# Performance work log

Measured on AMD Instinct MI355X. Metric: run time of the kernel, lower is better.

## Reference

```python
import jax, jax.numpy as jnp
import numpy as np

# Fixed architecture constants (match init_kwargs)
D_MODEL = 256
NHEAD = 8
BASE_WINDOW = 4
DFF = 1024
B = 1
S = 4096


def _win_idx(grid, w):
    """Token indices of overlapping w x w windows over a grid x grid image,
    stride w//2 (same windows as F.unfold(kernel=w, stride=w//2)). -> (L, w*w) int32."""
    s = w // 2
    starts = np.arange(0, grid - w + 1, s)
    rows = starts[:, None] + np.arange(w)[None, :]              # (n, w)
    idx = rows[:, None, :, None] * grid + rows[None, :, None, :]  # (n, n, w, w)
    return jnp.asarray(idx.reshape(-1, w * w), dtype=jnp.int32)


def _ln(x, g, b, eps=1e-5):
    m = jnp.mean(x, axis=-1, keepdims=True)
    v = jnp.var(x, axis=-1, keepdims=True)
    return (x - m) * jax.lax.rsqrt(v + eps) * g + b


def _local_attn(x, scale, fw, fb, fg, fbb):
    """Multi-scale windowed SDPA: gather windows, attend, mean-pool per window,
    scatter pooled features back to token positions (overlap-averaged), fuse."""
    Bq, Sq, Dm = x.shape
    grid = int(np.sqrt(Sq))
    inv_scale = 1.0 / float(np.sqrt(Dm))  # SDPA uses full D as head dim
    outs = []
    for i in range(3):
        w = BASE_WINDOW * (2 ** i) * scale
        idx = _win_idx(grid, w)                      # (L, w2)
        win = x[:, idx, :]                           # (B, L, w2, D) gather
        p = jax.nn.softmax(jnp.einsum('blqd,blkd->blqk', win, win) * inv_scale, axis=-1)
        pooled = jnp.einsum('blqk,blkd->blqd', p, win).mean(axis=2)  # (B, L, D)
        flat = idx.reshape(-1)
        contrib = jnp.broadcast_to(pooled[:, :, None, :], win.shape).reshape(Bq, -1, Dm)
        acc = jnp.zeros_like(x).at[:, flat, :].add(contrib)
        cnt = jnp.zeros((Sq,), x.dtype).at[flat].add(1.0)
        outs.append(acc / cnt[None, :, None])        # (B, S, D) per scale
    cat = jnp.concatenate(outs, axis=-1)             # (B, S, 3D)
    return _ln(cat @ fw + fb, fg, fbb)


def _mha(x, wq, wk, wv, bq, bk, bv, wo, bo):
    Bq, Sq, Dm = x.shape
    dh = Dm // NHEAD
    def split(t):
        return t.reshape(Bq, Sq, NHEAD, dh)
    q, k, v = split(x @ wq + bq), split(x @ wk + bk), split(x @ wv + bv)
    p = jax.nn.softmax(jnp.einsum('bqhd,bkhd->bhqk', q, k) * (1.0 / float(np.sqrt(dh))), axis=-1)
    o = jnp.einsum('bhqk,bkhd->bqhd', p, v).reshape(Bq, Sq, Dm)
    return o @ wo + bo


def _forward(x, pos, fw, fb, fg, fbb, wq, wk, wv, bq, bk, bv, wo, bo, gw, gb, w1, b1, w2, b2, n1g, n1b, n2g, n2b, n3g, n3b, local_scale):
    # pos is accepted but unused in the original math (device check only)
    xl = _local_attn(x, local_scale, fw, fb, fg, fbb)
    xl = _ln(x + xl, n1g, n1b)                 # norm1 residual (dropout is identity in eval)
    xg = _mha(xl, wq, wk, wv, bq, bk, bv, wo, bo)
    xg = _ln(xl + xg, n2g, n2b)                # norm2 residual
    gate = jax.nn.softmax(((xl + xg) * 0.5).mean(axis=1, keepdims=True) @ gw + gb, axis=-1)  # (B,1,2)
    alpha, beta = gate[..., 0:1], gate[..., 1:2]
    xf = alpha * xg + beta * xl
    ff = jax.nn.gelu(xf @ w1 + b1, approximate=False) @ w2 + b2
    return _ln(xf + ff, n3g, n3b)


def setup_inputs() -> dict:
    key = jax.random.key(0)
    ks = jax.random.split(key, 12)
    def rn(k, shape, s=0.02):
        return jax.random.normal(k, shape, jnp.float32) * s
    D = D_MODEL
    return {
        'x': jax.random.normal(ks[0], (B, S, D), jnp.float32),
        'pos': jax.random.normal(ks[1], (B, S, 2), jnp.float32),
        'fw': rn(ks[2], (3 * D, D)), 'fb': jnp.zeros((D,), jnp.float32),
        'fg': jnp.ones((D,), jnp.float32), 'fbb': jnp.zeros((D,), jnp.float32),
        'wq': rn(ks[3], (D, D)), 'wk': rn(ks[4], (D, D)), 'wv': rn(ks[5], (D, D)),
        'bq': jnp.zeros((D,), jnp.float32), 'bk': jnp.zeros((D,), jnp.float32), 'bv': jnp.zeros((D,), jnp.float32),
        'wo': rn(ks[6], (D, D)), 'bo': jnp.zeros((D,), jnp.float32),
        'gw': rn(ks[7], (D, 2)), 'gb': jnp.zeros((2,), jnp.float32),
        'w1': rn(ks[8], (D, DFF)), 'b1': jnp.zeros((DFF,), jnp.float32),
        'w2': rn(ks[9], (DFF, D)), 'b2': jnp.zeros((D,), jnp.float32),
        'n1g': jnp.ones((D,), jnp.float32), 'n1b': jnp.zeros((D,), jnp.float32),
        'n2g': jnp.ones((D,), jnp.float32), 'n2b': jnp.zeros((D,), jnp.float32),
        'n3g': jnp.ones((D,), jnp.float32), 'n3b': jnp.zeros((D,), jnp.float32),
        'local_scale': 1,
    }


def reference(x, pos, fw, fb, fg, fbb, wq, wk, wv, bq, bk, bv, wo, bo, gw, gb, w1, b1, w2, b2, n1g, n1b, n2g, n2b, n3g, n3b, local_scale):
    return _forward(x, pos, fw, fb, fg, fbb, wq, wk, wv, bq, bk, bv, wo, bo, gw, gb, w1, b1, w2, b2, n1g, n1b, n2g, n2b, n3g, n3b, local_scale)
```

## Files before the change

### kernel.cpp

```cpp
#include <hip/hip_runtime.h>
#include <hip/hip_bf16.h>
#include <cstdint>
#include <cstddef>


#define DEVFN __device__ __forceinline__

constexpr int S    = 4096;
constexpr int D    = 256;
constexpr int GRID = 64;
constexpr int NH   = 8;
constexpr int DH   = 32;

typedef __attribute__((ext_vector_type(8))) short bf16x8;
typedef __attribute__((ext_vector_type(4))) float f32x4;
typedef __attribute__((ext_vector_type(16))) float f32x16;
typedef __attribute__((ext_vector_type(2))) unsigned int u32x2;

DEVFN float asf(unsigned u) { return __uint_as_float(u); }

DEVFN unsigned short f2bf(float f) {
  unsigned u = __float_as_uint(f);
  u += 0x7fffu + ((u >> 16) & 1u);
  return (unsigned short)(u >> 16);
}
DEVFN float bf2f(unsigned short s) { return __uint_as_float(((unsigned)s) << 16); }

DEVFN unsigned pk2(float a, float b) {
  __hip_bfloat162 h = __float22bfloat162_rn(make_float2(a, b));
  return *(unsigned*)&h;
}

DEVFN bf16x8 pack8(float4 a, float4 b) {
  union { unsigned w[4]; bf16x8 v; } u;
  u.w[0] = pk2(a.x, a.y); u.w[1] = pk2(a.z, a.w);
  u.w[2] = pk2(b.x, b.y); u.w[3] = pk2(b.z, b.w);
  return u.v;
}

DEVFN float ex2(float x) {
#if __has_builtin(__builtin_amdgcn_exp2f)
  return __builtin_amdgcn_exp2f(x);
#else
  return __expf(x * 0.6931471805599453f);
#endif
}

DEVFN float gelu_t(float u) {
  const float y = 0.7978845608028654f * (u + 0.044715f * u * u * u);
  const float e = __expf(2.f * y);
  return 0.5f * u * (2.f - 2.f / (e + 1.f));
}

__global__ __launch_bounds__(256) void k_wt(
    const float* fw, const float* wq, const float* wk, const float* wv,
    const float* wo, const float* w1, const float* w2,
    unsigned short* fwT, unsigned short* wqT, unsigned short* wkT,
    unsigned short* wvT, unsigned short* woT, unsigned short* w1T,
    unsigned short* w2T) {
  __shared__ unsigned short tile[32][36];
  const int bid = blockIdx.x;
  const float* src; unsigned short* dst; int K, N, t;
  if (bid < 192)      { src = fw; dst = fwT; K = 768;  N = 256;  t = bid; }
  else if (bid < 256) { src = wq; dst = wqT; K = 256;  N = 256;  t = bid - 192; }
  else if (bid < 320) { src = wk; dst = wkT; K = 256;  N = 256;  t = bid - 256; }
  else if (bid < 384) { src = wv; dst = wvT; K = 256;  N = 256;  t = bid - 320; }
  else if (bid < 448) { src = wo; dst = woT; K = 256;  N = 256;  t = bid - 384; }
  else if (bid < 704) { src = w1; dst = w1T; K = 256;  N = 1024; t = bid - 448; }
  else                { src = w2; dst = w2T; K = 1024; N = 256;  t = bid - 704; }
  const int nkt = K >> 5;
  const int k0 = (t % nkt) * 32, n0 = (t / nkt) * 32;
  const int i = threadIdx.x >> 3, j4 = threadIdx.x & 7;
  const float4 v = *(const float4*)(src + (size_t)(k0 + i) * N + n0 + j4 * 4);
  *(uint2*)&tile[i][j4 * 4] = make_uint2(pk2(v.x, v.y), pk2(v.z, v.w));
  __syncthreads();
  unsigned o0 = tile[j4 * 4 + 0][i], o1 = tile[j4 * 4 + 1][i];
  unsigned o2 = tile[j4 * 4 + 2][i], o3 = tile[j4 * 4 + 3][i];
  *(uint2*)(dst + (size_t)(n0 + i) * K + k0 + j4 * 4) =
      make_uint2(o0 | (o1 << 16), o2 | (o3 << 16));
}

template <int K, int OUTBF, int ACT>
__global__ __launch_bounds__(64) void k_gemm_m(const unsigned short* __restrict__ Ab,
                                               const unsigned short* __restrict__ WT,
                                               const float* __restrict__ bias,
                                               void* __restrict__ Cout, int N) {
  const int lane = threadIdx.x;
  const int lc = lane & 31, hi = lane >> 5;
  const int m0 = blockIdx.x * 32, n0 = blockIdx.y * 32;
  const unsigned short* ap = Ab + (size_t)(m0 + lc) * K + hi * 8;
  const unsigned short* bp = WT + (size_t)(n0 + lc) * K + hi * 8;
  f32x16 acc0 = {0.f,0.f,0.f,0.f,0.f,0.f,0.f,0.f,0.f,0.f,0.f,0.f,0.f,0.f,0.f,0.f};
  f32x16 acc1 = acc0;
#pragma unroll 4
  for (int k0 = 0; k0 < K; k0 += 32) {
    bf16x8 a0 = *(const bf16x8*)(ap + k0);
    bf16x8 b0 = *(const bf16x8*)(bp + k0);
    bf16x8 a1 = *(const bf16x8*)(ap + k0 + 16);
    bf16x8 b1 = *(const bf16x8*)(bp + k0 + 16);
    acc0 = __builtin_amdgcn_mfma_f32_32x32x16_bf16(a0, b0, acc0, 0, 0, 0);
    acc1 = __builtin_amdgcn_mfma_f32_32x32x16_bf16(a1, b1, acc1, 0, 0, 0);
  }
  const float bv = bias[n0 + lc];
#pragma unroll
  for (int r = 0; r < 16; ++r) {
    const int row = (r & 3) + 8 * (r >> 2) + 4 * hi;
    float v = acc0[r] + acc1[r] + bv;
    if (ACT == 1) v = gelu_t(v);
    if (OUTBF) ((unsigned short*)Cout)[(size_t)(m0 + row) * N + n0 + lc] = f2bf(v);
    else       ((float*)Cout)[(size_t)(m0 + row) * N + n0 + lc] = v;
  }
}

__global__ __launch_bounds__(64) void k_gemm_qkv(const unsigned short* __restrict__ Ab,
                                                 const unsigned short* __restrict__ wqkvT,
                                                 const float* __restrict__ bq,
                                                 const float* __restrict__ bk,
                                                 const float* __restrict__ bv,
                                                 unsigned short* __restrict__ qb,
                                                 unsigned short* __restrict__ kb,
                                                 unsigned short* __restrict__ vb) {
  const int lane = threadIdx.x;
  const int lc = lane & 31, hi = lane >> 5;
  const int m0 = blockIdx.x * 32;
  const int sel = blockIdx.y >> 3, n0 = (blockIdx.y & 7) * 32;
  const unsigned short* WT = wqkvT + (size_t)sel * 256 * 256;
  const float* bias = sel == 0 ? bq : sel == 1 ? bk : bv;
  unsigned short* out = sel == 0 ? qb : sel == 1 ? kb : vb;
  const float oscale = sel == 0 ? 0.25505889254f : 1.f;
  const unsigned short* ap = Ab + (size_t)(m0 + lc) * 256 + hi * 8;
  const unsigned short* bp = WT + (size_t)(n0 + lc) * 256 + hi * 8;
  f32x16 acc0 = {0.f,0.f,0.f,0.f,0.f,0.f,0.f,0.f,0.f,0.f,0.f,0.f,0.f,0.f,0.f,0.f};
  f32x16 acc1 = acc0;
#pragma unroll 4
  for (int k0 = 0; k0 < 256; k0 += 32) {
    bf16x8 a0 = *(const bf16x8*)(ap + k0);
    bf16x8 b0 = *(const bf16x8*)(bp + k0);
    bf16x8 a1 = *(const bf16x8*)(ap + k0 + 16);
    bf16x8 b1 = *(const bf16x8*)(bp + k0 + 16);
    acc0 = __builtin_amdgcn_mfma_f32_32x32x16_bf16(a0, b0, acc0, 0, 0, 0);
    acc1 = __builtin_amdgcn_mfma_f32_32x32x16_bf16(a1, b1, acc1, 0, 0, 0);
  }
  const float bvv = bias[n0 + lc];
#pragma unroll
  for (int r = 0; r < 16; ++r) {
    const int row = (r & 3) + 8 * (r >> 2) + 4 * hi;
    out[(size_t)(m0 + row) * 256 + n0 + lc] = f2bf((acc0[r] + acc1[r] + bvv) * oscale);
  }
}

template <int W, int THREADS>
__global__ __launch_bounds__(THREADS) void k_local_s(const float* __restrict__ x,
                                                     float* __restrict__ pooled, int nS) {
  constexpr int NT  = W * W;
  constexpr int NCT = NT / 16;
  constexpr int LDE = 264;
  __shared__ unsigned short win[NT][LDE];
  __shared__ float a[NT];
  const int tid = threadIdx.x;
  const int wave = tid >> 6, lane = tid & 63;
  const int lr = lane & 15, lg = lane >> 4;
  const int l = blockIdx.x;
  const int row0 = (l / nS) * (W / 2), col0 = (l % nS) * (W / 2);

  for (int e8 = tid; e8 < NT * 32; e8 += THREADS) {
    const int t = e8 >> 5, c8 = (e8 & 31) * 8;
    const float* src = x + ((size_t)((row0 + t / W) * GRID + col0 + (t % W))) * D + c8;
    *(bf16x8*)&win[t][c8] = pack8(*(const float4*)src, *(const float4*)(src + 4));
  }
  if (tid < NT) a[tid] = 0.f;
  __syncthreads();

  bf16x8 af[8];
#pragma unroll
  for (int k2 = 0; k2 < 8; ++k2)
    af[k2] = *(const bf16x8*)&win[wave * 16 + lr][k2 * 32 + lg * 8];

  float m[4], Z[4], Zi[4];
#pragma unroll
  for (int r = 0; r < 4; ++r) { m[r] = -INFINITY; Z[r] = 0.f; }

  for (int ct = 0; ct < NCT; ++ct) {
    f32x4 Ca = {0.f, 0.f, 0.f, 0.f}, Cb = {0.f, 0.f, 0.f, 0.f};
#pragma unroll
    for (int k2 = 0; k2 < 8; k2 += 2) {
      bf16x8 b0 = *(const bf16x8*)&win[ct * 16 + lr][k2 * 32 + lg * 8];
      bf16x8 b1 = *(const bf16x8*)&win[ct * 16 + lr][(k2 + 1) * 32 + lg * 8];
      Ca = __builtin_amdgcn_mfma_f32_16x16x32_bf16(af[k2], b0, Ca, 0, 0, 0);
      Cb = __builtin_amdgcn_mfma_f32_16x16x32_bf16(af[k2 + 1], b1, Cb, 0, 0, 0);
    }
#pragma unroll
    for (int r = 0; r < 4; ++r) {
      const float sv = (Ca[r] + Cb[r]) * 0.0625f;
      const float nm = fmaxf(m[r], sv);
      Z[r] = Z[r] * __expf(m[r] - nm) + __expf(sv - nm);
      m[r] = nm;
    }
  }
#pragma unroll
  for (int r = 0; r < 4; ++r) {
#pragma unroll
    for (int msk = 1; msk <= 8; msk <<= 1) {
      const float om = __shfl_xor(m[r], msk), oz = __shfl_xor(Z[r], msk);
      const float nm = fmaxf(m[r], om);
      Z[r] = Z[r] * __expf(m[r] - nm) + oz * __expf(om - nm);
      m[r] = nm;
    }
    Zi[r] = 1.f / Z[r];
  }

  for (int ct = 0; ct < NCT; ++ct) {
    f32x4 Ca = {0.f, 0.f, 0.f, 0.f}, Cb = {0.f, 0.f, 0.f, 0.f};
#pragma unroll
    for (int k2 = 0; k2 < 8; k2 += 2) {
      bf16x8 b0 = *(const bf16x8*)&win[ct * 16 + lr][k2 * 32 + lg * 8];
      bf16x8 b1 = *(const bf16x8*)&win[ct * 16 + lr][(k2 + 1) * 32 + lg * 8];
      Ca = __builtin_amdgcn_mfma_f32_16x16x32_bf16(af[k2], b0, Ca, 0, 0, 0);
      Cb = __builtin_amdgcn_mfma_f32_16x16x32_bf16(af[k2 + 1], b1, Cb, 0, 0, 0);
    }
    float cs = 0.f;
#pragma unroll
    for (int r = 0; r < 4; ++r)
      cs += __expf((Ca[r] + Cb[r]) * 0.0625f - m[r]) * Zi[r];
    cs += __shfl_xor(cs, 16);
    cs += __shfl_xor(cs, 32);
    if (lg == 0) atomicAdd(&a[ct * 16 + lr], cs);
  }
  __syncthreads();

  for (int d = tid; d < D; d += THREADS) {
    float acc = 0.f;
#pragma unroll 8
    for (int k = 0; k < NT; ++k) acc += a[k] * bf2f(win[k][d]);
    pooled[(size_t)l * D + d] = acc * (1.f / NT);
  }
}

__global__ __launch_bounds__(256, 1) void k_local16(const float* __restrict__ x,
                                                    float* __restrict__ pooled, int nS) {
  constexpr int LDE = 264;
  __shared__ unsigned short win[256][LDE];
  __shared__ float a[256];
  const int tid = threadIdx.x;
  const int wave = tid >> 6, lane = tid & 63;
  const int lc = lane & 31, hi = lane >> 5;
  const int l = blockIdx.x;
  const int row0 = (l / nS) * 8, col0 = (l % nS) * 8;

  for (int e8 = tid; e8 < 256 * 32; e8 += 256) {
    const int t = e8 >> 5, c8 = (e8 & 31) * 8;
    const float* src = x + ((size_t)((row0 + (t >> 4)) * GRID + col0 + (t & 15))) * D + c8;
    *(bf16x8*)&win[t][c8] = pack8(*(const float4*)src, *(const float4*)(src + 4));
  }
  a[tid] = 0.f;
  __syncthreads();

  float m[2][16], Z[2][16], Zi[2][16];
#pragma unroll
  for (int s = 0; s < 2; ++s)
#pragma unroll
    for (int r = 0; r < 16; ++r) { m[s][r] = -INFINITY; Z[s][r] = 0.f; }

#pragma unroll
  for (int s = 0; s < 2; ++s) {
    const int R0 = (wave * 2 + s) * 32;
    bf16x8 af[16];
#pragma unroll
    for (int k2 = 0; k2 < 16; ++k2)
      af[k2] = *(const bf16x8*)&win[R0 + lc][k2 * 16 + hi * 8];
    for (int ct = 0; ct < 8; ++ct) {
      f32x16 Ca = {0.f,0.f,0.f,0.f,0.f,0.f,0.f,0.f,0.f,0.f,0.f,0.f,0.f,0.f,0.f,0.f};
      f32x16 Cb = Ca;
#pragma unroll
      for (int k2 = 0; k2 < 16; k2 += 2) {
        bf16x8 b0 = *(const bf16x8*)&win[ct * 32 + lc][k2 * 16 + hi * 8];
        bf16x8 b1 = *(const bf16x8*)&win[ct * 32 + lc][(k2 + 1) * 16 + hi * 8];
        Ca = __builtin_amdgcn_mfma_f32_32x32x16_bf16(af[k2], b0, Ca, 0, 0, 0);
        Cb = __builtin_amdgcn_mfma_f32_32x32x16_bf16(af[k2 + 1], b1, Cb, 0, 0, 0);
      }
#pragma unroll
      for (int r = 0; r < 16; ++r) {
        const float sv = (Ca[r] + Cb[r]) * 0.0625f;
        const float nm = fmaxf(m[s][r], sv);
        Z[s][r] = Z[s][r] * __expf(m[s][r] - nm) + __expf(sv - nm);
        m[s][r] = nm;
      }
    }
#pragma unroll
    for (int r = 0; r < 16; ++r) {
#pragma unroll
      for (int msk = 1; msk <= 16; msk <<= 1) {
        const float om = __shfl_xor(m[s][r], msk), oz = __shfl_xor(Z[s][r], msk);
        const float nm = fmaxf(m[s][r], om);
        Z[s][r] = Z[s][r] * __expf(m[s][r] - nm) + oz * __expf(om - nm);
        m[s][r] = nm;
      }
      Zi[s][r] = 1.f / Z[s][r];
    }
  }

#pragma unroll
  for (int s = 0; s < 2; ++s) {
    const int R0 = (wave * 2 + s) * 32;
    bf16x8 af[16];
#pragma unroll
    for (int k2 = 0; k2 < 16; ++k2)
      af[k2] = *(const bf16x8*)&win[R0 + lc][k2 * 16 + hi * 8];
    for (int ct = 0; ct < 8; ++ct) {
      f32x16 Ca = {0.f,0.f,0.f,0.f,0.f,0.f,0.f,0.f,0.f,0.f,0.f,0.f,0.f,0.f,0.f,0.f};
      f32x16 Cb = Ca;
#pragma unroll
      for (int k2 = 0; k2 < 16; k2 += 2) {
        bf16x8 b0 = *(const bf16x8*)&win[ct * 32 + lc][k2 * 16 + hi * 8];
        bf16x8 b1 = *(const bf16x8*)&win[ct * 32 + lc][(k2 + 1) * 16 + hi * 8];
        Ca = __builtin_amdgcn_mfma_f32_32x32x16_bf16(af[k2], b0, Ca, 0, 0, 0);
        Cb = __builtin_amdgcn_mfma_f32_32x32x16_bf16(af[k2 + 1], b1, Cb, 0, 0, 0);
      }
      float cs = 0.f;
#pragma unroll
      for (int r = 0; r < 16; ++r)
        cs += __expf((Ca[r] + Cb[r]) * 0.0625f - m[s][r]) * Zi[s][r];
      cs += __shfl_xor(cs, 32);
      if (hi == 0) atomicAdd(&a[ct * 32 + lc], cs);
    }
  }
  __syncthreads();

  {
    const int d = tid;
    float acc = 0.f;
#pragma unroll 8
    for (int k = 0; k < 256; ++k) acc += a[k] * bf2f(win[k][d]);
    pooled[(size_t)l * D + d] = acc * (1.f / 256.f);
  }
}

DEVFN float gatherp(const float* __restrict__ pooled, int r, int c, int W, int s, int nS, int d) {
  int amin = max(0, (r - W + s) / s), amax = min(nS - 1, r / s);
  int bmin = max(0, (c - W + s) / s), bmax = min(nS - 1, c / s);
  float acc = 0.f;
  int cnt = 0;
  for (int a = amin; a <= amax; ++a)
    for (int b = bmin; b <= bmax; ++b) { acc += pooled[(size_t)(a * nS + b) * D + d]; ++cnt; }
  return acc / (float)cnt;
}

__global__ void k_combine(const float* __restrict__ p0, const float* __restrict__ p1,
                          const float* __restrict__ p2, unsigned short* __restrict__ catb) {
  const int t = blockIdx.x, d = threadIdx.x;
  const int r = t >> 6, c = t & 63;
  unsigned short* o = catb + (size_t)t * 768;
  o[d]       = f2bf(gatherp(p0, r, c, 4, 2, 31, d));
  o[256 + d] = f2bf(gatherp(p1, r, c, 8, 4, 15, d));
  o[512 + d] = f2bf(gatherp(p2, r, c, 16, 8, 7, d));
}

DEVFN float2 block_sum2(float a, float b) {
  __shared__ float sb[8];
#pragma unroll
  for (int m = 32; m; m >>= 1) { a += __shfl_xor(a, m); b += __shfl_xor(b, m); }
  const int w = threadIdx.x >> 6;
  __syncthreads();
  if ((threadIdx.x & 63) == 0) { sb[w] = a; sb[4 + w] = b; }
  __syncthreads();
  return make_float2(sb[0] + sb[1] + sb[2] + sb[3], sb[4] + sb[5] + sb[6] + sb[7]);
}

__global__ __launch_bounds__(256) void k_ln(float* __restrict__ out, unsigned short* __restrict__ outb,
                                            const float* __restrict__ a, const float* __restrict__ b,
                                            const float* __restrict__ g, const float* __restrict__ be) {
  const size_t i = (size_t)blockIdx.x * D + threadIdx.x;
  float v = a[i] + (b ? b[i] : 0.f);
  float2 s = block_sum2(v, v * v);
  float mean = s.x * (1.f / D);
  float var = s.y * (1.f / D) - mean * mean;
  const float r = (v - mean) * rsqrtf(var + 1e-5f) * g[threadIdx.x] + be[threadIdx.x];
  out[i] = r;
  if (outb) outb[i] = f2bf(r);
}

__global__ __launch_bounds__(256) void k_ln_fuse(const float* __restrict__ t1,
                                                 const float* __restrict__ x,
                                                 float* __restrict__ xl,
                                                 unsigned short* __restrict__ xlb,
                                                 const float* __restrict__ fg,
                                                 const float* __restrict__ fbb,
                                                 const float* __restrict__ n1g,
                                                 const float* __restrict__ n1b) {
  const size_t i = (size_t)blockIdx.x * D + threadIdx.x;
  const float v1 = t1[i];
  float2 s1 = block_sum2(v1, v1 * v1);
  const float mean1 = s1.x * (1.f / D);
  const float var1 = s1.y * (1.f / D) - mean1 * mean1;
  const float r1 = (v1 - mean1) * rsqrtf(var1 + 1e-5f) * fg[threadIdx.x] + fbb[threadIdx.x];
  const float v2 = x[i] + r1;
  float2 s2 = block_sum2(v2, v2 * v2);
  const float mean2 = s2.x * (1.f / D);
  const float var2 = s2.y * (1.f / D) - mean2 * mean2;
  const float r2 = (v2 - mean2) * rsqrtf(var2 + 1e-5f) * n1g[threadIdx.x] + n1b[threadIdx.x];
  xl[i] = r2;
  xlb[i] = f2bf(r2);
}

__global__ __launch_bounds__(256) void k_flash_mfma(const unsigned short* __restrict__ Qg,
                                                    const unsigned short* __restrict__ Kg,
                                                    const unsigned short* __restrict__ Vg,
                                                    unsigned short* __restrict__ po,
                                                    float* __restrict__ pml) {
  const int h = blockIdx.y, z = blockIdx.z;
  const int tid = threadIdx.x;
  const int wave = tid >> 6, lane = tid & 63;
  const int lr = lane & 15, lg = lane >> 4;
  constexpr int NT2 = 16;

  __shared__ unsigned short Kf[2][64][40];
  __shared__ unsigned short VS[2][2048];

  const int q0 = blockIdx.x * 64 + wave * 16;
  const int kbase = z * 1024;

  const bf16x8 qfrag = *(const bf16x8*)(Qg + (size_t)(q0 + lr) * D + h * DH + lg * 8);

  f32x4 o0 = {0.f, 0.f, 0.f, 0.f}, o1 = {0.f, 0.f, 0.f, 0.f};
  float mrow = -INFINITY, lrow = 0.f;

  const unsigned vsbase0 =
      (unsigned)(unsigned long long)(const void*)&VS[0][0] + (unsigned)(lg * 128 + lr * 2);

  const int key = tid >> 2, c8 = (tid & 3) * 8;
  const int vidx = (c8 >> 4) * 1024 + (key >> 2) * 64 + (key & 3) * 16 + (c8 & 15);
  const unsigned short* kp = Kg + (size_t)(kbase + key) * D + h * DH + c8;
  const unsigned short* vp = Vg + (size_t)(kbase + key) * D + h * DH + c8;
  constexpr int KSTEP = 64 * D;

  {
    bf16x8 k0r = *(const bf16x8*)kp;
    bf16x8 v0r = *(const bf16x8*)vp;
    *(bf16x8*)&Kf[0][key][c8] = k0r;
    *(bf16x8*)&VS[0][vidx] = v0r;
  }
  __syncthreads();

  for (int kt = 0; kt < NT2; ++kt) {
    const int cur = kt & 1;
    const int ktn = (kt + 1 < NT2) ? kt + 1 : kt;
    bf16x8 kreg = *(const bf16x8*)(kp + (size_t)ktn * KSTEP);
    bf16x8 vreg = *(const bf16x8*)(vp + (size_t)ktn * KSTEP);

    f32x4 s[4];
    __builtin_amdgcn_s_setprio(1);
#pragma unroll
    for (int k16 = 0; k16 < 4; ++k16) {
      bf16x8 ka = *(const bf16x8*)&Kf[cur][k16 * 16 + lr][lg * 8];
      f32x4 zc = {0.f, 0.f, 0.f, 0.f};
      s[k16] = __builtin_amdgcn_mfma_f32_16x16x32_bf16(ka, qfrag, zc, 0, 0, 0);
    }
    __builtin_amdgcn_s_setprio(0);

    const unsigned vb = vsbase0 + (unsigned)(cur << 12);
    u32x2 tv000, tv001, tv010, tv011, tv100, tv101, tv110, tv111;
    asm volatile("ds_read_b64_tr_b16 %0, %1 offset:0"    : "=v"(tv000) : "v"(vb));
    asm volatile("ds_read_b64_tr_b16 %0, %1 offset:2048" : "=v"(tv001) : "v"(vb));
    asm volatile("ds_read_b64_tr_b16 %0, %1 offset:512"  : "=v"(tv010) : "v"(vb));
    asm volatile("ds_read_b64_tr_b16 %0, %1 offset:2560" : "=v"(tv011) : "v"(vb));
    asm volatile("ds_read_b64_tr_b16 %0, %1 offset:1024" : "=v"(tv100) : "v"(vb));
    asm volatile("ds_read_b64_tr_b16 %0, %1 offset:3072" : "=v"(tv101) : "v"(vb));
    asm volatile("ds_read_b64_tr_b16 %0, %1 offset:1536" : "=v"(tv110) : "v"(vb));
    asm volatile("ds_read_b64_tr_b16 %0, %1 offset:3584" : "=v"(tv111) : "v"(vb));

    float tm = s[0][0];
#pragma unroll
    for (int k16 = 0; k16 < 4; ++k16)
#pragma unroll
      for (int r = 0; r < 4; ++r) tm = fmaxf(tm, s[k16][r]);
    const bool skip = __all(tm - mrow <= 11.f);
    if (!skip) {
      float tmm = fmaxf(tm, __shfl_xor(tm, 16));
      tmm = fmaxf(tmm, __shfl_xor(tmm, 32));
      const float nm = fmaxf(mrow, tmm);
      const float cfac = ex2(mrow - nm);
      mrow = nm;
      lrow *= cfac;
#pragma unroll
      for (int r = 0; r < 4; ++r) {
        const float cr = __shfl(cfac, lg * 4 + r);
        o0[r] *= cr; o1[r] *= cr;
      }
    }
    float ls = 0.f;
#pragma unroll
    for (int k16 = 0; k16 < 4; ++k16)
#pragma unroll
      for (int r = 0; r < 4; ++r) { s[k16][r] = ex2(s[k16][r] - mrow); ls += s[k16][r]; }
    ls += __shfl_xor(ls, 16);
    ls += __shfl_xor(ls, 32);
    lrow += ls;

    asm volatile("s_waitcnt lgkmcnt(0)" ::: "memory");
    __builtin_amdgcn_sched_barrier(0);

    union VB { u32x2 u2[2]; bf16x8 b; };
    __builtin_amdgcn_s_setprio(1);
#pragma unroll
    for (int kt2 = 0; kt2 < 2; ++kt2) {
      union { unsigned w[4]; bf16x8 v; } pu;
      pu.w[0] = pk2(s[2 * kt2][0], s[2 * kt2][1]);
      pu.w[1] = pk2(s[2 * kt2][2], s[2 * kt2][3]);
      pu.w[2] = pk2(s[2 * kt2 + 1][0], s[2 * kt2 + 1][1]);
      pu.w[3] = pk2(s[2 * kt2 + 1][2], s[2 * kt2 + 1][3]);
      VB v0f, v1f;
      if (kt2 == 0) { v0f.u2[0] = tv000; v0f.u2[1] = tv010; v1f.u2[0] = tv001; v1f.u2[1] = tv011; }
      else          { v0f.u2[0] = tv100; v0f.u2[1] = tv110; v1f.u2[0] = tv101; v1f.u2[1] = tv111; }
      o0 = __builtin_amdgcn_mfma_f32_16x16x32_bf16(pu.v, v0f.b, o0, 0, 0, 0);
      o1 = __builtin_amdgcn_mfma_f32_16x16x32_bf16(pu.v, v1f.b, o1, 0, 0, 0);
    }
    __builtin_amdgcn_s_setprio(0);

    if (kt + 1 < NT2) {
      *(bf16x8*)&Kf[cur ^ 1][key][c8] = kreg;
      *(bf16x8*)&VS[cur ^ 1][vidx] = vreg;
      __syncthreads();
    }
  }

#pragma unroll
  for (int r = 0; r < 4; ++r) {
    unsigned short* op = po + (size_t)z * S * D + (size_t)(q0 + lg * 4 + r) * D + h * DH + lr;
    op[0]  = f2bf(o0[r]);
    op[16] = f2bf(o1[r]);
  }
  if (lane < 16) {
    float* mlp = pml + ((size_t)(z * NH + h) * S + q0 + lr) * 2;
    mlp[0] = mrow;
    mlp[1] = lrow;
  }
}

__global__ __launch_bounds__(256) void k_fmerge(const unsigned short* __restrict__ po,
                                                const float* __restrict__ pml,
                                                unsigned short* __restrict__ t1b) {
  const int t = blockIdx.x, d = threadIdx.x;
  const int h = d >> 5;
  float m[4], l[4];
  float M = -INFINITY;
#pragma unroll
  for (int z = 0; z < 4; ++z) {
    const float* ml = pml + ((size_t)(z * NH + h) * S + t) * 2;
    m[z] = ml[0]; l[z] = ml[1];
    M = fmaxf(M, m[z]);
  }
  float L = 0.f, acc = 0.f;
#pragma unroll
  for (int z = 0; z < 4; ++z) {
    const float a = ex2(m[z] - M);
    L += l[z] * a;
    acc += bf2f(po[(size_t)z * S * D + (size_t)t * D + d]) * a;
  }
  t1b[(size_t)t * D + d] = f2bf(acc / L);
}

__global__ __launch_bounds__(256) void k_colmean(const float* __restrict__ xl,
                                                 const float* __restrict__ xg,
                                                 float* __restrict__ gbuf) {
  const int j = threadIdx.x;
  const int t0 = blockIdx.x * 64;
  float s = 0.f;
  for (int t = 0; t < 64; ++t) {
    size_t i = (size_t)(t0 + t) * D + j;
    s += xl[i] + xg[i];
  }
  atomicAdd(&gbuf[j], s * 0.5f);
}

__global__ __launch_bounds__(256) void k_gate(float* __restrict__ gbuf,
                                              const float* __restrict__ gw,
                                              const float* __restrict__ gb) {
  const int j = threadIdx.x;
  const float gm = gbuf[j] * (1.f / (float)S);
  float2 s = block_sum2(gm * gw[2 * j], gm * gw[2 * j + 1]);
  if (j == 0) {
    float g0 = s.x + gb[0], g1 = s.y + gb[1];
    float mx = fmaxf(g0, g1);
    float e0 = __expf(g0 - mx), e1 = __expf(g1 - mx);
    gbuf[256] = e0 / (e0 + e1);
    gbuf[257] = e1 / (e0 + e1);
  }
}

__global__ __launch_bounds__(256) void k_xf(const float* __restrict__ xl,
                                            const float* __restrict__ xg,
                                            const float* __restrict__ gbuf,
                                            float* __restrict__ xf,
                                            unsigned short* __restrict__ xfb) {
  const float alpha = gbuf[256], beta = gbuf[257];
  const size_t i = ((size_t)blockIdx.x * 256 + threadIdx.x) * 4;
  float4 a = *(const float4*)(xg + i);
  float4 b = *(const float4*)(xl + i);
  float4 r;
  r.x = alpha * a.x + beta * b.x;
  r.y = alpha * a.y + beta * b.y;
  r.z = alpha * a.z + beta * b.z;
  r.w = alpha * a.w + beta * b.w;
  *(float4*)(xf + i) = r;
  *(uint2*)(xfb + i) = make_uint2(pk2(r.x, r.y), pk2(r.z, r.w));
}

extern "C" void kernel_launch(void* const* d_in, const int* in_sizes, int n_in,
                              void* d_out, int out_size, void* d_ws, size_t ws_size,
                              hipStream_t stream) {
  const float* x   = (const float*)d_in[0];
  const float* fw  = (const float*)d_in[2];
  const float* fb  = (const float*)d_in[3];
  const float* fg  = (const float*)d_in[4];
  const float* fbb = (const float*)d_in[5];
  const float* wq  = (const float*)d_in[6];
  const float* wk  = (const float*)d_in[7];
  const float* wv  = (const float*)d_in[8];
  const float* bq  = (const float*)d_in[9];
  const float* bk  = (const float*)d_in[10];
  const float* bv  = (const float*)d_in[11];
  const float* wo  = (const float*)d_in[12];
  const float* bo  = (const float*)d_in[13];
  const float* gw  = (const float*)d_in[14];
  const float* gb  = (const float*)d_in[15];
  const float* w1  = (const float*)d_in[16];
  const float* b1  = (const float*)d_in[17];
  const float* w2  = (const float*)d_in[18];
  const float* b2  = (const float*)d_in[19];
  const float* n1g = (const float*)d_in[20];
  const float* n1b = (const float*)d_in[21];
  const float* n2g = (const float*)d_in[22];
  const float* n2b = (const float*)d_in[23];
  const float* n3g = (const float*)d_in[24];
  const float* n3b = (const float*)d_in[25];
  float* out = (float*)d_out;

  char* base = (char*)d_ws;
  size_t off = 0;
  auto carve = [&](size_t bytes) { char* p = base + off; off += (bytes + 255) & ~(size_t)255; return p; };
  float* p0 = (float*)carve(961 * 256 * 4);
  float* p1 = (float*)carve(225 * 256 * 4);
  float* p2 = (float*)carve(49 * 256 * 4);
  unsigned short* fwT = (unsigned short*)carve(256 * 768 * 2);
  unsigned short* wqkvT = (unsigned short*)carve(3 * 256 * 256 * 2);
  unsigned short* wqT = wqkvT;
  unsigned short* wkT = wqkvT + 256 * 256;
  unsigned short* wvT = wqkvT + 2 * 256 * 256;
  unsigned short* woT = (unsigned short*)carve(256 * 256 * 2);
  unsigned short* w1T = (unsigned short*)carve(1024 * 256 * 2);
  unsigned short* w2T = (unsigned short*)carve(256 * 1024 * 2);
  char* R = carve(8388608);
  unsigned short* catb = (unsigned short*)R;
  unsigned short* po   = (unsigned short*)R;
  float* xg            = (float*)R;
  unsigned short* hbuf = (unsigned short*)R;
  float* pml = (float*)carve(4 * NH * (size_t)S * 2 * 4);
  unsigned short* qb = (unsigned short*)carve((size_t)S * D * 2);
  unsigned short* kb = (unsigned short*)carve((size_t)S * D * 2);
  unsigned short* vb = (unsigned short*)carve((size_t)S * D * 2);
  float* xf            = (float*)qb;
  unsigned short* xfb  = vb;
  float* t1  = (float*)carve((size_t)S * D * 4);
  float* ffo = t1;
  unsigned short* t1b = (unsigned short*)carve((size_t)S * D * 2);
  float* xl  = (float*)carve((size_t)S * D * 4);
  unsigned short* xlb = (unsigned short*)carve((size_t)S * D * 2);
  float* gbuf = (float*)carve(264 * 4);

  hipMemsetAsync(gbuf, 0, 264 * sizeof(float), stream);

  k_wt<<<dim3(960), dim3(256), 0, stream>>>(fw, wq, wk, wv, wo, w1, w2,
                                            fwT, wqT, wkT, wvT, woT, w1T, w2T);
  k_local_s<4, 64><<<dim3(961), dim3(64), 0, stream>>>(x, p0, 31);
  k_local_s<8, 256><<<dim3(225), dim3(256), 0, stream>>>(x, p1, 15);
  k_local16<<<dim3(49), dim3(256), 0, stream>>>(x, p2, 7);
  k_combine<<<dim3(S), dim3(256), 0, stream>>>(p0, p1, p2, catb);
  k_gemm_m<768, 0, 0><<<dim3(S / 32, 8), dim3(64), 0, stream>>>(catb, fwT, fb, t1, 256);
  k_ln_fuse<<<dim3(S), dim3(256), 0, stream>>>(t1, x, xl, xlb, fg, fbb, n1g, n1b);
  k_gemm_qkv<<<dim3(S / 32, 24), dim3(64), 0, stream>>>(xlb, wqkvT, bq, bk, bv, qb, kb, vb);
  k_flash_mfma<<<dim3(S / 64, NH, 4), dim3(256), 0, stream>>>(qb, kb, vb, po, pml);
  k_fmerge<<<dim3(S), dim3(256), 0, stream>>>(po, pml, t1b);
  k_gemm_m<256, 0, 0><<<dim3(S / 32, 8), dim3(64), 0, stream>>>(t1b, woT, bo, xf, 256);
  k_ln<<<dim3(S), dim3(256), 0, stream>>>(xg, nullptr, xl, xf, n2g, n2b);
  k_colmean<<<dim3(64), dim3(256), 0, stream>>>(xl, xg, gbuf);
  k_gate<<<dim3(1), dim3(256), 0, stream>>>(gbuf, gw, gb);
  k_xf<<<dim3(S * D / 1024), dim3(256), 0, stream>>>(xl, xg, gbuf, xf, xfb);
  k_gemm_m<256, 1, 1><<<dim3(S / 32, 32), dim3(64), 0, stream>>>(xfb, w1T, b1, hbuf, 1024);
  k_gemm_m<1024, 0, 0><<<dim3(S / 32, 8), dim3(64), 0, stream>>>(hbuf, w2T, b2, ffo, 256);
  k_ln<<<dim3(S), dim3(256), 0, stream>>>(out, nullptr, xf, ffo, n3g, n3b);
}
```

Before: 229.9 us.

## Split 16x16 window attention across two blocks, defer flash row-sum reduction, unroll GEMM K loops

The 16x16 local-window kernel now runs on a 2D grid: each block handles half of the 256 query rows, and pooled output is combined with global atomicAdds into a buffer that is zeroed beforehand. This doubles parallelism for a kernel that previously ran only 49 blocks on a large GPU. The cost is redundant window loading into shared memory and atomic traffic. The flash attention kernel moves the row-sum cross-lane shuffles out of the key loop to a single reduction at the end, and flattens the max computation into a tree. The GEMM K-loop unroll is raised from 4 to 8.

```diff
diff --git a/kernel.cpp b/kernel.cpp
--- a/kernel.cpp
+++ b/kernel.cpp
@@ -92,7 +92,7 @@
   const unsigned short* bp = WT + (size_t)(n0 + lc) * K + hi * 8;
   f32x16 acc0 = {0.f,0.f,0.f,0.f,0.f,0.f,0.f,0.f,0.f,0.f,0.f,0.f,0.f,0.f,0.f,0.f};
   f32x16 acc1 = acc0;
-#pragma unroll 4
+#pragma unroll 8
   for (int k0 = 0; k0 < K; k0 += 32) {
     bf16x8 a0 = *(const bf16x8*)(ap + k0);
     bf16x8 b0 = *(const bf16x8*)(bp + k0);
@@ -132,7 +132,7 @@
   const unsigned short* bp = WT + (size_t)(n0 + lc) * 256 + hi * 8;
   f32x16 acc0 = {0.f,0.f,0.f,0.f,0.f,0.f,0.f,0.f,0.f,0.f,0.f,0.f,0.f,0.f,0.f,0.f};
   f32x16 acc1 = acc0;
-#pragma unroll 4
+#pragma unroll 8
   for (int k0 = 0; k0 < 256; k0 += 32) {
     bf16x8 a0 = *(const bf16x8*)(ap + k0);
     bf16x8 b0 = *(const bf16x8*)(bp + k0);
@@ -244,7 +244,7 @@
   const int tid = threadIdx.x;
   const int wave = tid >> 6, lane = tid & 63;
   const int lc = lane & 31, hi = lane >> 5;
-  const int l = blockIdx.x;
+  const int l = blockIdx.x, z = blockIdx.y;
   const int row0 = (l / nS) * 8, col0 = (l % nS) * 8;
 
   for (int e8 = tid; e8 < 256 * 32; e8 += 256) {
@@ -255,74 +255,62 @@
   a[tid] = 0.f;
   __syncthreads();
 
-  float m[2][16], Z[2][16], Zi[2][16];
-#pragma unroll
-  for (int s = 0; s < 2; ++s)
-#pragma unroll
-    for (int r = 0; r < 16; ++r) { m[s][r] = -INFINITY; Z[s][r] = 0.f; }
-
-#pragma unroll
-  for (int s = 0; s < 2; ++s) {
-    const int R0 = (wave * 2 + s) * 32;
-    bf16x8 af[16];
-#pragma unroll
-    for (int k2 = 0; k2 < 16; ++k2)
-      af[k2] = *(const bf16x8*)&win[R0 + lc][k2 * 16 + hi * 8];
-    for (int ct = 0; ct < 8; ++ct) {
-      f32x16 Ca = {0.f,0.f,0.f,0.f,0.f,0.f,0.f,0.f,0.f,0.f,0.f,0.f,0.f,0.f,0.f,0.f};
-      f32x16 Cb = Ca;
-#pragma unroll
-      for (int k2 = 0; k2 < 16; k2 += 2) {
-        bf16x8 b0 = *(const bf16x8*)&win[ct * 32 + lc][k2 * 16 + hi * 8];
-        bf16x8 b1 = *(const bf16x8*)&win[ct * 32 + lc][(k2 + 1) * 16 + hi * 8];
-        Ca = __builtin_amdgcn_mfma_f32_32x32x16_bf16(af[k2], b0, Ca, 0, 0, 0);
-        Cb = __builtin_amdgcn_mfma_f32_32x32x16_bf16(af[k2 + 1], b1, Cb, 0, 0, 0);
-      }
-#pragma unroll
-      for (int r = 0; r < 16; ++r) {
-        const float sv = (Ca[r] + Cb[r]) * 0.0625f;
-        const float nm = fmaxf(m[s][r], sv);
-        Z[s][r] = Z[s][r] * __expf(m[s][r] - nm) + __expf(sv - nm);
-        m[s][r] = nm;
-      }
+  const int R0 = (z * 4 + wave) * 32;
+  bf16x8 af[16];
+#pragma unroll
+  for (int k2 = 0; k2 < 16; ++k2)
+    af[k2] = *(const bf16x8*)&win[R0 + lc][k2 * 16 + hi * 8];
+
+  float m[16], Z[16], Zi[16];
+#pragma unroll
+  for (int r = 0; r < 16; ++r) { m[r] = -INFINITY; Z[r] = 0.f; }
+
+  for (int ct = 0; ct < 8; ++ct) {
+    f32x16 Ca = {0.f,0.f,0.f,0.f,0.f,0.f,0.f,0.f,0.f,0.f,0.f,0.f,0.f,0.f,0.f,0.f};
+    f32x16 Cb = Ca;
+#pragma unroll
+    for (int k2 = 0; k2 < 16; k2 += 2) {
+      bf16x8 b0 = *(const bf16x8*)&win[ct * 32 + lc][k2 * 16 + hi * 8];
+      bf16x8 b1 = *(const bf16x8*)&win[ct * 32 + lc][(k2 + 1) * 16 + hi * 8];
+      Ca = __builtin_amdgcn_mfma_f32_32x32x16_bf16(af[k2], b0, Ca, 0, 0, 0);
+      Cb = __builtin_amdgcn_mfma_f32_32x32x16_bf16(af[k2 + 1], b1, Cb, 0, 0, 0);
     }
 #pragma unroll
     for (int r = 0; r < 16; ++r) {
-#pragma unroll
-      for (int msk = 1; msk <= 16; msk <<= 1) {
-        const float om = __shfl_xor(m[s][r], msk), oz = __shfl_xor(Z[s][r], msk);
-        const float nm = fmaxf(m[s][r], om);
-        Z[s][r] = Z[s][r] * __expf(m[s][r] - nm) + oz * __expf(om - nm);
-        m[s][r] = nm;
-      }
-      Zi[s][r] = 1.f / Z[s][r];
-    }
-  }
-
-#pragma unroll
-  for (int s = 0; s < 2; ++s) {
-    const int R0 = (wave * 2 + s) * 32;
-    bf16x8 af[16];
-#pragma unroll
-    for (int k2 = 0; k2 < 16; ++k2)
-      af[k2] = *(const bf16x8*)&win[R0 + lc][k2 * 16 + hi * 8];
-    for (int ct = 0; ct < 8; ++ct) {
-      f32x16 Ca = {0.f,0.f,0.f,0.f,0.f,0.f,0.f,0.f,0.f,0.f,0.f,0.f,0.f,0.f,0.f,0.f};
-      f32x16 Cb = Ca;
-#pragma unroll
-      for (int k2 = 0; k2 < 16; k2 += 2) {
-        bf16x8 b0 = *(const bf16x8*)&win[ct * 32 + lc][k2 * 16 + hi * 8];
-        bf16x8 b1 = *(const bf16x8*)&win[ct * 32 + lc][(k2 + 1) * 16 + hi * 8];
-        Ca = __builtin_amdgcn_mfma_f32_32x32x16_bf16(af[k2], b0, Ca, 0, 0, 0);
-        Cb = __builtin_amdgcn_mfma_f32_32x32x16_bf16(af[k2 + 1], b1, Cb, 0, 0, 0);
-      }
-      float cs = 0.f;
-#pragma unroll
-      for (int r = 0; r < 16; ++r)
-        cs += __expf((Ca[r] + Cb[r]) * 0.0625f - m[s][r]) * Zi[s][r];
-      cs += __shfl_xor(cs, 32);
-      if (hi == 0) atomicAdd(&a[ct * 32 + lc], cs);
-    }
+      const float sv = (Ca[r] + Cb[r]) * 0.0625f;
+      const float nm = fmaxf(m[r], sv);
+      Z[r] = Z[r] * __expf(m[r] - nm) + __expf(sv - nm);
+      m[r] = nm;
+    }
+  }
+#pragma unroll
+  for (int r = 0; r < 16; ++r) {
+#pragma unroll
+    for (int msk = 1; msk <= 16; msk <<= 1) {
+      const float om = __shfl_xor(m[r], msk), oz = __shfl_xor(Z[r], msk);
+      const float nm = fmaxf(m[r], om);
+      Z[r] = Z[r] * __expf(m[r] - nm) + oz * __expf(om - nm);
+      m[r] = nm;
+    }
+    Zi[r] = 1.f / Z[r];
+  }
+
+  for (int ct = 0; ct < 8; ++ct) {
+    f32x16 Ca = {0.f,0.f,0.f,0.f,0.f,0.f,0.f,0.f,0.f,0.f,0.f,0.f,0.f,0.f,0.f,0.f};
+    f32x16 Cb = Ca;
+#pragma unroll
+    for (int k2 = 0; k2 < 16; k2 += 2) {
+      bf16x8 b0 = *(const bf16x8*)&win[ct * 32 + lc][k2 * 16 + hi * 8];
+      bf16x8 b1 = *(const bf16x8*)&win[ct * 32 + lc][(k2 + 1) * 16 + hi * 8];
+      Ca = __builtin_amdgcn_mfma_f32_32x32x16_bf16(af[k2], b0, Ca, 0, 0, 0);
+      Cb = __builtin_amdgcn_mfma_f32_32x32x16_bf16(af[k2 + 1], b1, Cb, 0, 0, 0);
+    }
+    float cs = 0.f;
+#pragma unroll
+    for (int r = 0; r < 16; ++r)
+      cs += __expf((Ca[r] + Cb[r]) * 0.0625f - m[r]) * Zi[r];
+    cs += __shfl_xor(cs, 32);
+    if (hi == 0) atomicAdd(&a[ct * 32 + lc], cs);
   }
   __syncthreads();
 
@@ -331,7 +319,7 @@
     float acc = 0.f;
 #pragma unroll 8
     for (int k = 0; k < 256; ++k) acc += a[k] * bf2f(win[k][d]);
-    pooled[(size_t)l * D + d] = acc * (1.f / 256.f);
+    atomicAdd(&pooled[(size_t)l * D + d], acc * (1.f / 256.f));
   }
 }
 
@@ -468,11 +456,10 @@
     asm volatile("ds_read_b64_tr_b16 %0, %1 offset:1536" : "=v"(tv110) : "v"(vb));
     asm volatile("ds_read_b64_tr_b16 %0, %1 offset:3584" : "=v"(tv111) : "v"(vb));
 
-    float tm = s[0][0];
-#pragma unroll
-    for (int k16 = 0; k16 < 4; ++k16)
-#pragma unroll
-      for (int r = 0; r < 4; ++r) tm = fmaxf(tm, s[k16][r]);
+    float tm = fmaxf(fmaxf(fmaxf(s[0][0], s[0][1]), fmaxf(s[0][2], s[0][3])),
+                     fmaxf(fmaxf(s[1][0], s[1][1]), fmaxf(s[1][2], s[1][3])));
+    tm = fmaxf(tm, fmaxf(fmaxf(fmaxf(s[2][0], s[2][1]), fmaxf(s[2][2], s[2][3])),
+                         fmaxf(fmaxf(s[3][0], s[3][1]), fmaxf(s[3][2], s[3][3]))));
     const bool skip = __all(tm - mrow <= 11.f);
     if (!skip) {
       float tmm = fmaxf(tm, __shfl_xor(tm, 16));
@@ -487,14 +474,10 @@
         o0[r] *= cr; o1[r] *= cr;
       }
     }
-    float ls = 0.f;
 #pragma unroll
     for (int k16 = 0; k16 < 4; ++k16)
 #pragma unroll
-      for (int r = 0; r < 4; ++r) { s[k16][r] = ex2(s[k16][r] - mrow); ls += s[k16][r]; }
-    ls += __shfl_xor(ls, 16);
-    ls += __shfl_xor(ls, 32);
-    lrow += ls;
+      for (int r = 0; r < 4; ++r) { s[k16][r] = ex2(s[k16][r] - mrow); lrow += s[k16][r]; }
 
     asm volatile("s_waitcnt lgkmcnt(0)" ::: "memory");
     __builtin_amdgcn_sched_barrier(0);
@@ -522,6 +505,9 @@
       __syncthreads();
     }
   }
+
+  lrow += __shfl_xor(lrow, 16);
+  lrow += __shfl_xor(lrow, 32);
 
 #pragma unroll
   for (int r = 0; r < 4; ++r) {
@@ -668,12 +654,13 @@
   float* gbuf = (float*)carve(264 * 4);
 
   hipMemsetAsync(gbuf, 0, 264 * sizeof(float), stream);
+  hipMemsetAsync(p2, 0, 49 * 256 * sizeof(float), stream);
 
   k_wt<<<dim3(960), dim3(256), 0, stream>>>(fw, wq, wk, wv, wo, w1, w2,
                                             fwT, wqT, wkT, wvT, woT, w1T, w2T);
   k_local_s<4, 64><<<dim3(961), dim3(64), 0, stream>>>(x, p0, 31);
   k_local_s<8, 256><<<dim3(225), dim3(256), 0, stream>>>(x, p1, 15);
-  k_local16<<<dim3(49), dim3(256), 0, stream>>>(x, p2, 7);
+  k_local16<<<dim3(49, 2), dim3(256), 0, stream>>>(x, p2, 7);
   k_combine<<<dim3(S), dim3(256), 0, stream>>>(p0, p1, p2, catb);
   k_gemm_m<768, 0, 0><<<dim3(S / 32, 8), dim3(64), 0, stream>>>(catb, fwT, fb, t1, 256);
   k_ln_fuse<<<dim3(S), dim3(256), 0, stream>>>(t1, x, xl, xlb, fg, fbb, n1g, n1b);
```

Measured after the change: 213.7 us. 1.08x faster.
